# Optimization experiments

Hardware: AMD Instinct MI355X
Metric: run time of the kernel (lower is better)

The kernel has to match this reference:

```python
import jax, jax.numpy as jnp
import numpy as np

B, N, L, E, U, G, R, D, C = 64, 50000, 8, 100000, 20000, 20000, 64, 16, 2


def setup_inputs() -> dict:
    rng = np.random.default_rng(0)
    key = jax.random.key(0)
    ks = jax.random.split(key, 10)
    # index structures (duplicate-free where the torch code assumes uniqueness)
    gene_map = jnp.asarray(rng.choice(N, G, replace=False).astype(np.int32))
    dst_unique = jnp.stack([jnp.asarray(rng.choice(N, U, replace=False).astype(np.int32)) for _ in range(L)])
    root_ids = jnp.asarray(rng.choice(N, R, replace=False).astype(np.int32))
    src = jax.random.randint(ks[0], (L, E), 0, N, dtype=jnp.int32)
    dst_pos = jax.random.randint(ks[1], (L, E), 0, U, dtype=jnp.int32)
    # data and parameters
    X_gene_batch = jax.random.normal(ks[2], (B, G), jnp.float32)
    w_in = jax.random.normal(ks[3], (D,), jnp.float32) * 0.5   # Linear(1, d) weight
    b_in = jax.random.normal(ks[4], (D,), jnp.float32) * 0.1
    W = jax.random.normal(ks[5], (L, D, D), jnp.float32) * (1.0 / np.sqrt(D))  # xavier-ish
    bias = jnp.zeros((N, D), jnp.float32)
    W_head = jax.random.normal(ks[6], (C, R * D), jnp.float32) * (1.0 / np.sqrt(R * D))
    b_head = jnp.zeros((C,), jnp.float32)
    return {
        "X_gene_batch": X_gene_batch, "w_in": w_in, "b_in": b_in, "W": W,
        "bias": bias, "W_head": W_head, "b_head": b_head,
        "gene_map": gene_map, "src": src, "dst_pos": dst_pos,
        "dst_unique": dst_unique, "root_ids": root_ids,
    }


def reference(X_gene_batch, w_in, b_in, W, bias, W_head, b_head,
              gene_map, src, dst_pos, dst_unique, root_ids):
    Bn = X_gene_batch.shape[0]
    n_nodes, d = bias.shape
    n_layers = W.shape[0]
    u = dst_unique.shape[1]
    # _init_state_vector: h=0, scatter in_proj(X[...,None]) at gene_map
    gene_emb = X_gene_batch[..., None] * w_in + b_in          # [B, G, d]
    h = jnp.zeros((Bn, n_nodes, d), X_gene_batch.dtype)
    h = h.at[:, gene_map].set(gene_emb)
    for li in range(n_layers):
        h_src = h[:, src[li]]                                  # gather [B, E, d]
        msg = jnp.einsum('bed,df->bef', h_src, W[li])          # small dxd matmul
        agg = jnp.zeros((Bn, u, d), h.dtype).at[:, dst_pos[li]].add(msg)  # scatter-add
        h_dst = jnp.tanh(agg + bias[dst_unique[li]][None])     # bias lookup + tanh (dropout=0)
        h = h.at[:, dst_unique[li]].set(h_dst)                 # write back
    feat = h[:, root_ids].reshape(Bn, -1)                      # roots_concat readout
    return feat @ W_head.T + b_head                            # [B, C]
```

## Files before the change

kernel.cpp:

```cpp
#include <hip/hip_runtime.h>
#include <hip/hip_fp16.h>
#include <cmath>

constexpr int B_ = 64, N_ = 50000, L_ = 8, E_ = 100000, U_ = 20000, G_ = 20000, R_ = 64, D_ = 16, C_ = 2;
constexpr int EPL_ = E_ + 3 * U_ + 4096;
constexpr int EPLG_ = EPL_ / 4 + 16;
constexpr int GPW = 8;
constexpr int BC = 64;
constexpr int F = BC * 2;


__device__ __forceinline__ float tanh_fast(float x) {
  float e = __expf(2.0f * x);
  return 1.0f - 2.0f * __builtin_amdgcn_rcpf(e + 1.0f);
}


__global__ __launch_bounds__(256) void hist_kernel(
    const int* __restrict__ dst_pos, int* __restrict__ cnt,
    int* __restrict__ rank) {
  int e = blockIdx.x * 256 + threadIdx.x;
  int li = blockIdx.y;
  if (e >= E_) return;
  rank[li * E_ + e] = atomicAdd(&cnt[li * U_ + dst_pos[li * E_ + e]], 1);
}

__global__ __launch_bounds__(1024) void scan_kernel(
    const int* __restrict__ cnt, int* __restrict__ offs) {
  __shared__ int sums[1024];
  int li = blockIdx.x, t = threadIdx.x;
  int base = t * 20;
  int v[20];
  int s = 0;
#pragma unroll
  for (int i = 0; i < 20; ++i) {
    int idx = base + i;
    int c = (idx < U_) ? cnt[li * U_ + idx] : -1;
    int pc = (c < 0) ? 0 : ((c == 0) ? 4 : ((c + 3) & ~3));
    v[i] = s;
    s += pc;
  }
  sums[t] = s;
  __syncthreads();
  for (int off = 1; off < 1024; off <<= 1) {
    int o = (t >= off) ? sums[t - off] : 0;
    __syncthreads();
    sums[t] += o;
    __syncthreads();
  }
  int excl = sums[t] - s;
#pragma unroll
  for (int i = 0; i < 20; ++i) {
    int idx = base + i;
    if (idx < U_) offs[li * (U_ + 1) + idx] = excl + v[i];
  }
  if (t == 1023) offs[li * (U_ + 1) + U_] = sums[1023];
}

__global__ __launch_bounds__(256) void scatter_kernel(
    const int* __restrict__ dst_pos, const int* __restrict__ src,
    const int* __restrict__ offs, const int* __restrict__ rank,
    int* __restrict__ ssrc) {
  int e = blockIdx.x * 256 + threadIdx.x;
  int li = blockIdx.y;
  if (e >= E_) return;
  int u = dst_pos[li * E_ + e];
  int p = offs[li * (U_ + 1) + u] + rank[li * E_ + e];
  ssrc[(size_t)li * EPL_ + p] = src[li * E_ + e];
}

__global__ __launch_bounds__(256) void pad_fill_ug_k(
    const int* __restrict__ cnt, const int* __restrict__ offs,
    int* __restrict__ ssrc, int* __restrict__ ug) {
  int t = blockIdx.x * 256 + threadIdx.x;
  if (t >= L_ * U_) return;
  int li = t / U_, u = t % U_;
  int start = offs[li * (U_ + 1) + u];
  int end = start + cnt[li * U_ + u];
  int pend = offs[li * (U_ + 1) + u + 1];
  int* sp = ssrc + (size_t)li * EPL_;
  for (int p = end; p < pend; ++p) sp[p] = N_;
  int* ugp = ug + (size_t)li * EPLG_;
  for (int g = start >> 2; g < (pend >> 2); ++g) ugp[g] = u;
  if (u == U_ - 1) {
    int ptot = offs[li * (U_ + 1) + U_];
    for (int p = ptot; p < ptot + 8; ++p) sp[p] = N_;
  }
}


__global__ __launch_bounds__(256) void gene_init_k(
    const float* __restrict__ X, const float* __restrict__ w_in,
    const float* __restrict__ b_in, const int* __restrict__ gene_map,
    float4* __restrict__ h4) {
  int t = blockIdx.x * 256 + threadIdx.x;
  if (t >= G_ * BC) return;
  int b = t % BC;
  int g = t / BC;
  float x = X[b * G_ + g];
  int node = gene_map[g];
  float4 out[2];
  __half2* oh = reinterpret_cast<__half2*>(out);
#pragma unroll
  for (int k = 0; k < 8; ++k) {
    float r0 = fmaf(x, w_in[2 * k], b_in[2 * k]);
    float r1 = fmaf(x, w_in[2 * k + 1], b_in[2 * k + 1]);
    oh[k] = __float22half2_rn(make_float2(r0, r1));
  }
  h4[(size_t)node * F + b * 2] = out[0];
  h4[(size_t)node * F + b * 2 + 1] = out[1];
}

__global__ __launch_bounds__(256) void gather_k(
    const float4* __restrict__ h4, const int* __restrict__ ug,
    const int* __restrict__ ssrc, float4* __restrict__ agg4, int li) {
  int tid = threadIdx.x;
  int wave = tid >> 6, lane = tid & 63;
  int wv = blockIdx.x * 4 + wave;
  int g0 = wv * GPW, gend = g0 + GPW;
  const int* ugp = ug + (size_t)li * EPLG_;
  const int* sp = ssrc + (size_t)li * EPL_;

  int prevU = (g0 == 0) ? -2 : ugp[g0 - 1];
  int g = g0;
  while (g < gend && ugp[g] == prevU) ++g;
  if (g >= gend) return;
  int curU = ugp[g];
  if (curU < 0) return;

  __half2 acc[2][2][4];
  const __half2 z = __half2half2(__float2half(0.f));
#pragma unroll
  for (int j = 0; j < 2; ++j)
#pragma unroll
    for (int r = 0; r < 2; ++r)
#pragma unroll
      for (int k = 0; k < 4; ++k) acc[j][r][k] = z;

  auto flushu = [&](int u) {
#pragma unroll
    for (int r = 0; r < 2; ++r) {
      float4 outv;
      __half2* ov = reinterpret_cast<__half2*>(&outv);
#pragma unroll
      for (int k = 0; k < 4; ++k) {
        float2 f0 = __half22float2(acc[0][r][k]);
        float2 f1 = __half22float2(acc[1][r][k]);
        ov[k] = __float22half2_rn(make_float2(f0.x + f1.x, f0.y + f1.y));
      }
      agg4[(size_t)u * F + lane + r * 64] = outv;
    }
#pragma unroll
    for (int j = 0; j < 2; ++j)
#pragma unroll
      for (int r = 0; r < 2; ++r)
#pragma unroll
        for (int k = 0; k < 4; ++k) acc[j][r][k] = z;
  };

  auto loadRows = [&](float4 (&v)[4][2], int4 id) {
    v[0][0] = h4[(size_t)id.x * F + lane]; v[0][1] = h4[(size_t)id.x * F + lane + 64];
    v[1][0] = h4[(size_t)id.y * F + lane]; v[1][1] = h4[(size_t)id.y * F + lane + 64];
    v[2][0] = h4[(size_t)id.z * F + lane]; v[2][1] = h4[(size_t)id.z * F + lane + 64];
    v[3][0] = h4[(size_t)id.w * F + lane]; v[3][1] = h4[(size_t)id.w * F + lane + 64];
  };
  auto accum = [&](const float4 (&v)[4][2]) {
#pragma unroll
    for (int j = 0; j < 4; ++j)
#pragma unroll
      for (int r = 0; r < 2; ++r) {
        const __half2* p = reinterpret_cast<const __half2*>(&v[j][r]);
#pragma unroll
        for (int k = 0; k < 4; ++k)
          acc[j & 1][r][k] = __hadd2(acc[j & 1][r][k], p[k]);
      }
  };

  float4 va[4][2], vb[4][2];
  int4 idA = *(const int4*)(sp + 4 * g);
  loadRows(va, idA);
  int nuA = ugp[g + 1];
  int nuB;

  for (;;) {
    {
      bool more = (nuA >= 0) && ((nuA == curU) || (g + 1 < gend));
      if (more) {
        int4 idB = *(const int4*)(sp + 4 * (g + 1));
        loadRows(vb, idB);
        nuB = ugp[g + 2];
      }
      accum(va);
      if (nuA != curU) {
        flushu(curU);
        if (!more) return;
        curU = nuA;
      }
      ++g;
    }
    {
      bool more = (nuB >= 0) && ((nuB == curU) || (g + 1 < gend));
      if (more) {
        int4 idA2 = *(const int4*)(sp + 4 * (g + 1));
        loadRows(va, idA2);
        nuA = ugp[g + 2];
      }
      accum(vb);
      if (nuB != curU) {
        flushu(curU);
        if (!more) return;
        curU = nuB;
      }
      ++g;
    }
  }
}

__global__ __launch_bounds__(256) void dense_k(
    const float4* __restrict__ agg4, const float* __restrict__ W,
    const float* __restrict__ bias, const int* __restrict__ dst_unique,
    float4* __restrict__ h4, int li) {
  __shared__ float Wlds[256];
  int tid = threadIdx.x;
  Wlds[tid] = W[li * 256 + tid];
  __syncthreads();
  int t = blockIdx.x * 256 + tid;
  int u = t >> 6, b = t & 63;
  float4 c0 = agg4[(size_t)u * F + b * 2];
  float4 c1 = agg4[(size_t)u * F + b * 2 + 1];
  float a[16];
  {
    const __half2* p0 = reinterpret_cast<const __half2*>(&c0);
    const __half2* p1 = reinterpret_cast<const __half2*>(&c1);
#pragma unroll
    for (int k = 0; k < 4; ++k) {
      float2 f0 = __half22float2(p0[k]);
      float2 f1 = __half22float2(p1[k]);
      a[2 * k] = f0.x; a[2 * k + 1] = f0.y;
      a[8 + 2 * k] = f1.x; a[8 + 2 * k + 1] = f1.y;
    }
  }
  float m[16];
#pragma unroll
  for (int j = 0; j < 16; ++j) m[j] = 0.f;
#pragma unroll
  for (int d = 0; d < 16; ++d) {
    float s = a[d];
    const float4* wr = (const float4*)&Wlds[d * 16];
    float4 w0 = wr[0], w1 = wr[1], w2 = wr[2], w3 = wr[3];
    m[0] = fmaf(s, w0.x, m[0]);  m[1] = fmaf(s, w0.y, m[1]);
    m[2] = fmaf(s, w0.z, m[2]);  m[3] = fmaf(s, w0.w, m[3]);
    m[4] = fmaf(s, w1.x, m[4]);  m[5] = fmaf(s, w1.y, m[5]);
    m[6] = fmaf(s, w1.z, m[6]);  m[7] = fmaf(s, w1.w, m[7]);
    m[8] = fmaf(s, w2.x, m[8]);  m[9] = fmaf(s, w2.y, m[9]);
    m[10] = fmaf(s, w2.z, m[10]); m[11] = fmaf(s, w2.w, m[11]);
    m[12] = fmaf(s, w3.x, m[12]); m[13] = fmaf(s, w3.y, m[13]);
    m[14] = fmaf(s, w3.z, m[14]); m[15] = fmaf(s, w3.w, m[15]);
  }
  int node = dst_unique[li * U_ + u];
  const float4* bp = (const float4*)(bias + (size_t)node * 16);
  float4 b0 = bp[0], b1 = bp[1], b2 = bp[2], b3 = bp[3];
  float bb[16] = {b0.x, b0.y, b0.z, b0.w, b1.x, b1.y, b1.z, b1.w,
                  b2.x, b2.y, b2.z, b2.w, b3.x, b3.y, b3.z, b3.w};
  float4 o0, o1;
  __half2* ov0 = reinterpret_cast<__half2*>(&o0);
  __half2* ov1 = reinterpret_cast<__half2*>(&o1);
#pragma unroll
  for (int k = 0; k < 4; ++k) {
    ov0[k] = __float22half2_rn(make_float2(tanh_fast(m[2 * k] + bb[2 * k]),
                                           tanh_fast(m[2 * k + 1] + bb[2 * k + 1])));
    ov1[k] = __float22half2_rn(make_float2(tanh_fast(m[8 + 2 * k] + bb[8 + 2 * k]),
                                           tanh_fast(m[8 + 2 * k + 1] + bb[8 + 2 * k + 1])));
  }
  h4[(size_t)node * F + b * 2] = o0;
  h4[(size_t)node * F + b * 2 + 1] = o1;
}

__global__ __launch_bounds__(64) void head_k(
    const float4* __restrict__ h4, const float* __restrict__ W_head,
    const float* __restrict__ b_head, const int* __restrict__ root_ids,
    float* __restrict__ out) {
  int bl = blockIdx.x;
  int r = threadIdx.x;
  int node = root_ids[r];
  float4 p0 = h4[(size_t)node * F + bl * 2];
  float4 p1 = h4[(size_t)node * F + bl * 2 + 1];
  float v[16];
  const __half2* ph0 = reinterpret_cast<const __half2*>(&p0);
  const __half2* ph1 = reinterpret_cast<const __half2*>(&p1);
#pragma unroll
  for (int k = 0; k < 4; ++k) {
    float2 f0 = __half22float2(ph0[k]);
    float2 f1 = __half22float2(ph1[k]);
    v[2 * k] = f0.x; v[2 * k + 1] = f0.y;
    v[8 + 2 * k] = f1.x; v[8 + 2 * k + 1] = f1.y;
  }
  float acc0 = 0.f, acc1 = 0.f;
#pragma unroll
  for (int d = 0; d < 16; ++d) {
    acc0 = fmaf(v[d], W_head[r * 16 + d], acc0);
    acc1 = fmaf(v[d], W_head[1024 + r * 16 + d], acc1);
  }
  for (int off = 32; off; off >>= 1) {
    acc0 += __shfl_down(acc0, off, 64);
    acc1 += __shfl_down(acc1, off, 64);
  }
  if (r == 0) {
    out[bl * 2 + 0] = acc0 + b_head[0];
    out[bl * 2 + 1] = acc1 + b_head[1];
  }
}

__global__ void zero_out_k(float* out, int n) {
  int t = blockIdx.x * 256 + threadIdx.x;
  if (t < n) out[t] = 0.f;
}


static size_t need_bytes() {
  return (size_t)(N_ + 1) * F * 16 + (size_t)U_ * F * 16 +
         (size_t)L_ * U_ * 4 +
         (size_t)L_ * (U_ + 1) * 4 +
         (size_t)L_ * E_ * 4 +
         (size_t)L_ * EPL_ * 4;
}

extern "C" void kernel_launch(void* const* d_in, const int* in_sizes, int n_in,
                              void* d_out, int out_size, void* d_ws, size_t ws_size,
                              hipStream_t stream) {
  if (ws_size < need_bytes()) {
    zero_out_k<<<(out_size + 255) / 256, 256, 0, stream>>>((float*)d_out, out_size);
    return;
  }
  const float* X = (const float*)d_in[0];
  const float* w_in = (const float*)d_in[1];
  const float* b_in = (const float*)d_in[2];
  const float* W = (const float*)d_in[3];
  const float* bias = (const float*)d_in[4];
  const float* W_head = (const float*)d_in[5];
  const float* b_head = (const float*)d_in[6];
  const int* gene_map = (const int*)d_in[7];
  const int* src = (const int*)d_in[8];
  const int* dst_pos = (const int*)d_in[9];
  const int* dst_unique = (const int*)d_in[10];
  const int* root_ids = (const int*)d_in[11];
  float* out = (float*)d_out;

  const size_t h_bytes = (size_t)(N_ + 1) * F * 16;
  const size_t agg_bytes = (size_t)U_ * F * 16;
  const size_t cnt_bytes = (size_t)L_ * U_ * 4;
  const size_t offs_bytes = (size_t)L_ * (U_ + 1) * 4;
  const size_t rank_bytes = (size_t)L_ * E_ * 4;
  const size_t ug_bytes = (size_t)L_ * EPLG_ * 4;

  char* ws = (char*)d_ws;
  float4* h4 = (float4*)ws;
  float4* agg4 = (float4*)(ws + h_bytes);
  int* cnt = (int*)(ws + h_bytes + agg_bytes);
  int* offs = (int*)(ws + h_bytes + agg_bytes + cnt_bytes);
  int* rank = (int*)(ws + h_bytes + agg_bytes + cnt_bytes + offs_bytes);
  int* ug = rank;
  int* ssrc = (int*)(ws + h_bytes + agg_bytes + cnt_bytes + offs_bytes + rank_bytes);
  (void)ug_bytes;

  hipMemsetAsync(cnt, 0, cnt_bytes, stream);
  hipMemsetAsync(h4, 0, h_bytes, stream);
  dim3 egrid((E_ + 255) / 256, L_);
  hist_kernel<<<egrid, 256, 0, stream>>>(dst_pos, cnt, rank);
  scan_kernel<<<L_, 1024, 0, stream>>>(cnt, offs);
  scatter_kernel<<<egrid, 256, 0, stream>>>(dst_pos, src, offs, rank, ssrc);
  hipMemsetAsync(ug, 0xFF, ug_bytes, stream);
  pad_fill_ug_k<<<(L_ * U_ + 255) / 256, 256, 0, stream>>>(cnt, offs, ssrc, ug);

  gene_init_k<<<(G_ * BC + 255) / 256, 256, 0, stream>>>(X, w_in, b_in, gene_map, h4);

  const int total_groups = EPL_ / 4;
  const int gwaves = (total_groups + GPW - 1) / GPW;
  const int gather_grid = (gwaves + 3) / 4;
  const int dense_grid = U_ * BC / 256;
  for (int li = 0; li < L_; ++li) {
    gather_k<<<gather_grid, 256, 0, stream>>>(h4, ug, ssrc, agg4, li);
    dense_k<<<dense_grid, 256, 0, stream>>>(agg4, W, bias, dst_unique, h4, li);
  }

  head_k<<<BC, 64, 0, stream>>>(h4, W_head, b_head, root_ids, out);
}
```

Baseline: 626.9 us.

## Precompute gather span starts, halve groups per wave, tile gene init transpose

Adds a kernel that precomputes, for every wave span of edge groups, the first group index and destination it owns, so the per-layer gather kernel no longer scans ug at startup. Groups per wave drop from 8 to 4, doubling the gather grid for finer load balance. The gene init kernel now transposes X through shared memory so each wave writes whole node rows with coalesced loads and stores. In exchange there is an extra launch plus a span table in workspace, and more, shorter waves that each carry fixed overhead.

```diff
diff --git a/kernel.cpp b/kernel.cpp
--- a/kernel.cpp
+++ b/kernel.cpp
@@ -4,8 +4,10 @@
 
 constexpr int B_ = 64, N_ = 50000, L_ = 8, E_ = 100000, U_ = 20000, G_ = 20000, R_ = 64, D_ = 16, C_ = 2;
 constexpr int EPL_ = E_ + 3 * U_ + 4096;
-constexpr int EPLG_ = EPL_ / 4 + 16;
-constexpr int GPW = 8;
+constexpr int NGRP_ = EPL_ / 4;
+constexpr int EPLG_ = NGRP_ + 16;
+constexpr int GPW = 4;
+constexpr int NSPAN_ = (NGRP_ + GPW - 1) / GPW;
 constexpr int BC = 64;
 constexpr int F = BC * 2;
 
@@ -88,45 +90,72 @@
   }
 }
 
+__global__ __launch_bounds__(256) void spanstart_k(
+    const int* __restrict__ ug, int2* __restrict__ spantab) {
+  int t = blockIdx.x * 256 + threadIdx.x;
+  if (t >= L_ * NSPAN_) return;
+  int li = t / NSPAN_, w = t % NSPAN_;
+  const int* ugp = ug + (size_t)li * EPLG_;
+  int g0 = w * GPW, gend = g0 + GPW;
+  int prevU = (g0 == 0) ? -2 : ugp[g0 - 1];
+  int g = g0;
+  while (g < gend && ugp[g] == prevU) ++g;
+  int cu = (g < gend) ? ugp[g] : -1;
+  spantab[t] = (g < gend && cu >= 0) ? make_int2(g, cu) : make_int2(-1, -1);
+}
+
 
 __global__ __launch_bounds__(256) void gene_init_k(
     const float* __restrict__ X, const float* __restrict__ w_in,
     const float* __restrict__ b_in, const int* __restrict__ gene_map,
     float4* __restrict__ h4) {
-  int t = blockIdx.x * 256 + threadIdx.x;
-  if (t >= G_ * BC) return;
-  int b = t % BC;
-  int g = t / BC;
-  float x = X[b * G_ + g];
-  int node = gene_map[g];
-  float4 out[2];
-  __half2* oh = reinterpret_cast<__half2*>(out);
-#pragma unroll
-  for (int k = 0; k < 8; ++k) {
-    float r0 = fmaf(x, w_in[2 * k], b_in[2 * k]);
-    float r1 = fmaf(x, w_in[2 * k + 1], b_in[2 * k + 1]);
-    oh[k] = __float22half2_rn(make_float2(r0, r1));
-  }
-  h4[(size_t)node * F + b * 2] = out[0];
-  h4[(size_t)node * F + b * 2 + 1] = out[1];
+  __shared__ float xt[64][65];
+  int t = threadIdx.x;
+  int g0 = blockIdx.x * 64;
+  int col = t & 63, rowb = t >> 6;
+#pragma unroll
+  for (int i = 0; i < 16; ++i) {
+    int b = i * 4 + rowb;
+    int g = g0 + col;
+    xt[col][b] = (g < G_) ? X[b * G_ + g] : 0.f;
+  }
+  __syncthreads();
+  float wv[16], bv[16];
+#pragma unroll
+  for (int k = 0; k < 16; ++k) { wv[k] = w_in[k]; bv[k] = b_in[k]; }
+  int wave = t >> 6, lane = t & 63;
+#pragma unroll
+  for (int i = 0; i < 16; ++i) {
+    int g = g0 + wave * 16 + i;
+    if (g >= G_) break;
+    float x = xt[g - g0][lane];
+    int node = gene_map[g];
+    float4 out[2];
+    __half2* oh = reinterpret_cast<__half2*>(out);
+#pragma unroll
+    for (int k = 0; k < 8; ++k) {
+      float r0 = fmaf(x, wv[2 * k], bv[2 * k]);
+      float r1 = fmaf(x, wv[2 * k + 1], bv[2 * k + 1]);
+      oh[k] = __float22half2_rn(make_float2(r0, r1));
+    }
+    h4[(size_t)node * F + lane * 2] = out[0];
+    h4[(size_t)node * F + lane * 2 + 1] = out[1];
+  }
 }
 
 __global__ __launch_bounds__(256) void gather_k(
     const float4* __restrict__ h4, const int* __restrict__ ug,
-    const int* __restrict__ ssrc, float4* __restrict__ agg4, int li) {
+    const int2* __restrict__ spantab, const int* __restrict__ ssrc,
+    float4* __restrict__ agg4, int li) {
   int tid = threadIdx.x;
   int wave = tid >> 6, lane = tid & 63;
   int wv = blockIdx.x * 4 + wave;
-  int g0 = wv * GPW, gend = g0 + GPW;
+  int2 sc = spantab[li * NSPAN_ + wv];
+  if (sc.x < 0) return;
+  int g = sc.x, curU = sc.y;
+  int gend = wv * GPW + GPW;
   const int* ugp = ug + (size_t)li * EPLG_;
   const int* sp = ssrc + (size_t)li * EPL_;
-
-  int prevU = (g0 == 0) ? -2 : ugp[g0 - 1];
-  int g = g0;
-  while (g < gend && ugp[g] == prevU) ++g;
-  if (g >= gend) return;
-  int curU = ugp[g];
-  if (curU < 0) return;
 
   __half2 acc[2][2][4];
   const __half2 z = __half2half2(__float2half(0.f));
@@ -352,6 +381,7 @@
   const size_t offs_bytes = (size_t)L_ * (U_ + 1) * 4;
   const size_t rank_bytes = (size_t)L_ * E_ * 4;
   const size_t ug_bytes = (size_t)L_ * EPLG_ * 4;
+  const size_t stab_bytes = (size_t)L_ * NSPAN_ * 8;
 
   char* ws = (char*)d_ws;
   float4* h4 = (float4*)ws;
@@ -360,8 +390,9 @@
   int* offs = (int*)(ws + h_bytes + agg_bytes + cnt_bytes);
   int* rank = (int*)(ws + h_bytes + agg_bytes + cnt_bytes + offs_bytes);
   int* ug = rank;
+  int2* spantab = (int2*)((char*)rank + ug_bytes);
   int* ssrc = (int*)(ws + h_bytes + agg_bytes + cnt_bytes + offs_bytes + rank_bytes);
-  (void)ug_bytes;
+  (void)stab_bytes;
 
   hipMemsetAsync(cnt, 0, cnt_bytes, stream);
   hipMemsetAsync(h4, 0, h_bytes, stream);
@@ -371,15 +402,14 @@
   scatter_kernel<<<egrid, 256, 0, stream>>>(dst_pos, src, offs, rank, ssrc);
   hipMemsetAsync(ug, 0xFF, ug_bytes, stream);
   pad_fill_ug_k<<<(L_ * U_ + 255) / 256, 256, 0, stream>>>(cnt, offs, ssrc, ug);
-
-  gene_init_k<<<(G_ * BC + 255) / 256, 256, 0, stream>>>(X, w_in, b_in, gene_map, h4);
-
-  const int total_groups = EPL_ / 4;
-  const int gwaves = (total_groups + GPW - 1) / GPW;
-  const int gather_grid = (gwaves + 3) / 4;
+  spanstart_k<<<(L_ * NSPAN_ + 255) / 256, 256, 0, stream>>>(ug, spantab);
+
+  gene_init_k<<<(G_ + 63) / 64, 256, 0, stream>>>(X, w_in, b_in, gene_map, h4);
+
+  const int gather_grid = (NSPAN_ + 3) / 4;
   const int dense_grid = U_ * BC / 256;
   for (int li = 0; li < L_; ++li) {
-    gather_k<<<gather_grid, 256, 0, stream>>>(h4, ug, ssrc, agg4, li);
+    gather_k<<<gather_grid, 256, 0, stream>>>(h4, ug, spantab, ssrc, agg4, li);
     dense_k<<<dense_grid, 256, 0, stream>>>(agg4, W, bias, dst_unique, h4, li);
   }
 
```

After: 631.1 us. No clear change (+0.7%).
